# Kernel optimization log

Measured on AMD Instinct MI355X. Metric: run time of the kernel, lower is better.

Reference implementation:

```python
import jax, jax.numpy as jnp
import numpy as np
import math

B, T, C = 2, 4096, 768
NH = 12
HS = C // NH

def setup_inputs() -> dict:
    key = jax.random.key(0)
    k1, k2, k3 = jax.random.split(key, 3)
    x = jax.random.normal(k1, (B, T, C), dtype=jnp.float32)
    w_attn = jax.random.normal(k2, (C, 3 * C), dtype=jnp.float32) * (1.0 / math.sqrt(C))
    w_proj = jax.random.normal(k3, (C, C), dtype=jnp.float32) * (1.0 / math.sqrt(C))
    return {"x": x, "w_attn": w_attn, "w_proj": w_proj}

def reference(x, w_attn, w_proj):
    b, t, c = x.shape
    qkv = x @ w_attn                      # [b, t, 3c]
    q, k, v = jnp.split(qkv, 3, axis=-1)
    # [b, nh, t, hs]
    q = q.reshape(b, t, NH, HS).transpose(0, 2, 1, 3)
    k = k.reshape(b, t, NH, HS).transpose(0, 2, 1, 3)
    v = v.reshape(b, t, NH, HS).transpose(0, 2, 1, 3)
    scores = jnp.einsum('bhqd,bhkd->bhqk', q, k) / math.sqrt(HS)
    causal = jnp.tril(jnp.ones((t, t), dtype=bool))
    scores = jnp.where(causal[None, None], scores, -jnp.inf)
    att = jax.nn.softmax(scores, axis=-1)  # dropout p=0 -> identity
    out = jnp.einsum('bhqk,bhkd->bhqd', att, v)
    out = out.transpose(0, 2, 1, 3).reshape(b, t, c)
    return out @ w_proj
```

## Files before the change

kernel.cpp:

```cpp
#include <hip/hip_runtime.h>
#include <hip/hip_bf16.h>
#include <stdint.h>

#define NB 2
#define NT 4096
#define NC 768
#define NHEAD 12
#define HS 64
#define MTOK (NB * NT)
#define C3 (3 * NC)

typedef __bf16 bf16x8 __attribute__((ext_vector_type(8)));
typedef float f32x4 __attribute__((ext_vector_type(4)));
typedef float f32x16 __attribute__((ext_vector_type(16)));

#define KSCALE_LOG2E 0.18033688011f

__device__ __forceinline__ unsigned short f2bf(float f) {
  union { float f; uint32_t u; } v; v.f = f;
  uint32_t r = v.u + 0x7fffu + ((v.u >> 16) & 1u);
  return (unsigned short)(r >> 16);
}
__device__ __forceinline__ unsigned short bft(float f) {
  return (unsigned short)(__builtin_bit_cast(unsigned int, f) >> 16);
}
__device__ __forceinline__ uint32_t pack_bf2(float a, float b) {
  return __builtin_amdgcn_perm(__builtin_bit_cast(uint32_t, a),
                               __builtin_bit_cast(uint32_t, b), 0x03020706u);
}

__device__ __forceinline__ void gload_lds16(const unsigned short* g, unsigned short* ldsbase) {
  __builtin_amdgcn_global_load_lds(
      (const __attribute__((address_space(1))) unsigned int*)g,
      (__attribute__((address_space(3))) unsigned int*)ldsbase, 16, 0, 0);
}

__device__ __forceinline__ f32x4 mfma16(bf16x8 a, bf16x8 b, f32x4 c) {
  return __builtin_amdgcn_mfma_f32_16x16x32_bf16(a, b, c, 0, 0, 0);
}
__device__ __forceinline__ f32x16 mfma32(bf16x8 a, bf16x8 b, f32x16 c) {
  return __builtin_amdgcn_mfma_f32_32x32x16_bf16(a, b, c, 0, 0, 0);
}

__global__ __launch_bounds__(256) void prep(
    const float* __restrict__ x, const float* __restrict__ wa, const float* __restrict__ wp,
    unsigned short* __restrict__ xb, unsigned short* __restrict__ waT,
    unsigned short* __restrict__ wpT) {
  const int bx = blockIdx.x;
  if (bx < 576) {
    __shared__ float tile[64][65];
    const float* src; unsigned short* dst;
    int srcN, dstN, k0, n0, qscale;
    if (bx < 432) {
      src = wa; dst = waT; srcN = C3; dstN = NC; qscale = 1;
      k0 = (bx / 36) * 64; n0 = (bx % 36) * 64;
    } else {
      const int t = bx - 432;
      src = wp; dst = wpT; srcN = NC; dstN = NC; qscale = 0;
      k0 = (t / 12) * 64; n0 = (t % 12) * 64;
    }
    const int tr = threadIdx.x >> 4;
    const int tc = (threadIdx.x & 15) * 4;
#pragma unroll
    for (int p = 0; p < 4; ++p) {
      const int r = p * 16 + tr;
      const float4 v = *reinterpret_cast<const float4*>(src + (size_t)(k0 + r) * srcN + n0 + tc);
      tile[r][tc + 0] = v.x; tile[r][tc + 1] = v.y;
      tile[r][tc + 2] = v.z; tile[r][tc + 3] = v.w;
    }
    __syncthreads();
#pragma unroll
    for (int p = 0; p < 4; ++p) {
      const int n = p * 16 + tr;
      const float sc = (qscale && (n0 + n) < NC) ? KSCALE_LOG2E : 1.0f;
      ushort4 o;
      o.x = f2bf(tile[tc + 0][n] * sc); o.y = f2bf(tile[tc + 1][n] * sc);
      o.z = f2bf(tile[tc + 2][n] * sc); o.w = f2bf(tile[tc + 3][n] * sc);
      *reinterpret_cast<ushort4*>(dst + (size_t)(n0 + n) * dstN + k0 + tc) = o;
    }
  } else {
    const int gid = (bx - 576) * 256 + threadIdx.x;
    const float4 v = reinterpret_cast<const float4*>(x)[gid];
    ushort4 o;
    o.x = f2bf(v.x); o.y = f2bf(v.y); o.z = f2bf(v.z); o.w = f2bf(v.w);
    reinterpret_cast<ushort4*>(xb)[gid] = o;
  }
}

template <int OUT_BF16>
__global__ __launch_bounds__(256) void gemm128(
    const unsigned short* __restrict__ A,
    const unsigned short* __restrict__ Bt,
    void* __restrict__ Cout,
    unsigned short* __restrict__ vT,
    int M, int N, int K) {
  __shared__ unsigned short smem[2 * 128 * 64];
  unsigned short* As = smem;
  unsigned short* Bs = smem + 128 * 64;

  const int tid = threadIdx.x;
  const int wave = tid >> 6;
  const int lane = tid & 63;
  const int li = lane & 15;
  const int lq = lane >> 4;
  const int wm = wave & 1;
  const int wn = wave >> 1;
  const int row0 = blockIdx.y * 128;
  const int col0 = blockIdx.x * 128;

  const int crow = lane >> 3;
  const int cchunk = ((lane & 7) ^ crow) * 8;

  f32x4 acc[4][4] = {};

  for (int k0 = 0; k0 < K; k0 += 64) {
#pragma unroll
    for (int i = 0; i < 4; ++i) {
      const int R = wave * 32 + i * 8;
      gload_lds16(A + (size_t)(row0 + R + crow) * K + k0 + cchunk, &As[R * 64]);
      gload_lds16(Bt + (size_t)(col0 + R + crow) * K + k0 + cchunk, &Bs[R * 64]);
    }
    __syncthreads();

#pragma unroll
    for (int ks = 0; ks < 2; ++ks) {
      bf16x8 af[4], bf[4];
#pragma unroll
      for (int f = 0; f < 4; ++f) {
        const int arow = wm * 64 + f * 16 + li;
        af[f] = *reinterpret_cast<const bf16x8*>(&As[arow * 64 + (((ks * 4 + lq) ^ (li & 7)) << 3)]);
        const int brow = wn * 64 + f * 16 + li;
        bf[f] = *reinterpret_cast<const bf16x8*>(&Bs[brow * 64 + (((ks * 4 + lq) ^ (li & 7)) << 3)]);
      }
#pragma unroll
      for (int fa = 0; fa < 4; ++fa)
#pragma unroll
        for (int fb = 0; fb < 4; ++fb)
          acc[fa][fb] = mfma16(af[fa], bf[fb], acc[fa][fb]);
    }
    __syncthreads();
  }

  if (OUT_BF16) {
    if (col0 >= 2 * NC) {
      const int b = row0 >> 12;
      const int t0r = row0 & (NT - 1);
      const int h0 = (col0 - 2 * NC) >> 6;
#pragma unroll
      for (int fa = 0; fa < 4; ++fa) {
#pragma unroll
        for (int fb = 0; fb < 4; ++fb) {
          const int cc = wn * 64 + fb * 16 + li;
#pragma unroll
          for (int r = 0; r < 4; ++r) {
            const int tt = wm * 64 + fa * 16 + lq * 4 + r;
            const int slot = cc * 16 + ((tt >> 3) ^ (cc & 15));
            smem[slot * 8 + (tt & 7)] = f2bf(acc[fa][fb][r]);
          }
        }
      }
      __syncthreads();
      const int ch = tid & 15;
#pragma unroll
      for (int j = 0; j < 8; ++j) {
        const int cc = (tid >> 4) + 16 * j;
        const uint4 v = *reinterpret_cast<const uint4*>(
            smem + (size_t)(cc * 16 + (ch ^ (cc & 15))) * 8);
        const int bh = b * NHEAD + h0 + (cc >> 6);
        const int d = cc & 63;
        *reinterpret_cast<uint4*>(vT + (size_t)bh * HS * NT + (size_t)d * NT + t0r + ch * 8) = v;
      }
    } else {
      unsigned short* Cb = (unsigned short*)Cout;
#pragma unroll
      for (int fa = 0; fa < 4; ++fa) {
        const int gr = row0 + wm * 64 + fa * 16 + lq * 4;
#pragma unroll
        for (int fb = 0; fb < 4; ++fb) {
          const int gc = col0 + wn * 64 + fb * 16 + li;
#pragma unroll
          for (int r = 0; r < 4; ++r)
            Cb[(size_t)(gr + r) * N + gc] = f2bf(acc[fa][fb][r]);
        }
      }
    }
  } else {
    float* Cf = (float*)Cout;
#pragma unroll
    for (int fa = 0; fa < 4; ++fa) {
      const int gr = row0 + wm * 64 + fa * 16 + lq * 4;
#pragma unroll
      for (int fb = 0; fb < 4; ++fb) {
        const int gc = col0 + wn * 64 + fb * 16 + li;
#pragma unroll
        for (int r = 0; r < 4; ++r)
          Cf[(size_t)(gr + r) * N + gc] = acc[fa][fb][r];
      }
    }
  }
}


__device__ const uint8_t g_items[48] = {
  95,127,15, 94,126, 93,125,14, 92,124, 91,123,13, 90,122, 89,121,12, 88,120,
  87,119,11, 86,118, 85,117,10, 84,116, 83,115,9, 82,114, 81,113,8, 80,112,
  7,6,5,4,3,2,1,0};

__global__ __launch_bounds__(256) void attn(
    const unsigned short* __restrict__ qkv,
    const unsigned short* __restrict__ vT,
    float* __restrict__ Oacc,
    float* __restrict__ lacc,
    unsigned short* __restrict__ aob) {
  __shared__ unsigned short Ks[3][64 * 64];
  __shared__ unsigned short Vts[3][64 * 64];

  const int tid = threadIdx.x;
  const int wave = tid >> 6;
  const int lane = tid & 63;
  const int l31 = lane & 31;
  const int lh = lane >> 5;
  const int sw = l31 & 7;

  const int bid = (int)blockIdx.x;
  const int xcd = bid & 7;
  const int wl = bid >> 3;
  const int grp = xcd * 3 + wl % 3;
  const int e = (int)g_items[wl / 3];
  const int qi = e & 31;
  const int part = (e >> 5) & 1;
  const int split = e >> 6;
  const int nt = 2 * qi + 2;
  int tauS, tauE;
  if (split) { if (part) { tauS = nt >> 1; tauE = nt; } else { tauS = 0; tauE = nt >> 1; } }
  else       { tauS = 0; tauE = nt; }
  const int b = grp / 12;
  const int h = grp - b * 12;
  const int q0 = qi * 128;
  const int bh = grp;

  const size_t baseQ = (size_t)b * NT * C3 + (size_t)h * HS;
  const size_t baseK = baseQ + NC;
  const unsigned short* kq = qkv + baseK;
  const unsigned short* vbase = vT + (size_t)bh * HS * NT;

  const int qw = q0 + wave * 32;
  const int qtok = qw + l31;

  bf16x8 bq[4];
#pragma unroll
  for (int ks = 0; ks < 4; ++ks)
    bq[ks] = *reinterpret_cast<const bf16x8*>(
        qkv + baseQ + (size_t)(qw + l31) * C3 + ks * 16 + lh * 8);

  bf16x8 vones;
#pragma unroll
  for (int i = 0; i < 8; ++i) vones[i] = (__bf16)1.0f;

  f32x16 o0 = {}, o1 = {}, la = {};
  const f32x16 zf = {};

  const int grow = lane >> 3;
  const int gch = (lane & 7) ^ grow;
  const int wr0 = wave * 8;
  const int wr1 = wave * 8 + 32;

#define STAGE(TAU, BUFI)                                                        \
  do {                                                                          \
    const int t0s_ = (TAU) * 64;                                                \
    gload_lds16(kq + (size_t)(t0s_ + wr0 + grow) * C3 + gch * 8,                \
                &Ks[BUFI][wr0 * 64]);                                           \
    gload_lds16(kq + (size_t)(t0s_ + wr1 + grow) * C3 + gch * 8,                \
                &Ks[BUFI][wr1 * 64]);                                           \
    gload_lds16(vbase + (size_t)(wr0 + grow) * NT + t0s_ + gch * 8,             \
                &Vts[BUFI][wr0 * 64]);                                          \
    gload_lds16(vbase + (size_t)(wr1 + grow) * NT + t0s_ + gch * 8,             \
                &Vts[BUFI][wr1 * 64]);                                          \
  } while (0)

#define EXP_PACK(ST, KBLK, DOMASK)                                             \
  do {                                                                         \
    const int kb_ = t0 + (KBLK) * 32 + 4 * lh;                                 \
    float p_[16];                                                              \
    _Pragma("unroll") for (int r = 0; r < 16; ++r) {                           \
      float v_ = (ST)[r];                                                      \
      if (DOMASK) {                                                            \
        const int kt_ = kb_ + (r & 3) + 8 * (r >> 2);                          \
        if (kt_ > qtok) v_ = -INFINITY;                                        \
      }                                                                        \
      p_[r] = __builtin_amdgcn_exp2f(v_);                                      \
    }                                                                          \
    _Pragma("unroll") for (int s = 0; s < 2; ++s) {                            \
      uint32_t a_ = pack_bf2(p_[8 * s + 0], p_[8 * s + 1]);                    \
      uint32_t b_ = pack_bf2(p_[8 * s + 2], p_[8 * s + 3]);                    \
      uint32_t c_ = pack_bf2(p_[8 * s + 4], p_[8 * s + 5]);                    \
      uint32_t d_ = pack_bf2(p_[8 * s + 6], p_[8 * s + 7]);                    \
      asm("v_permlane32_swap_b32 %0, %1" : "+v"(a_), "+v"(c_));                \
      asm("v_permlane32_swap_b32 %0, %1" : "+v"(b_), "+v"(d_));                \
      union { uint32_t u[4]; bf16x8 v8; } pu_;                                 \
      pu_.u[0] = a_; pu_.u[1] = b_; pu_.u[2] = c_; pu_.u[3] = d_;              \
      pa[2 * (KBLK) + s] = pu_.v8;                                             \
    }                                                                          \
  } while (0)

#define PV_STEP(KS)                                                            \
  do {                                                                         \
    const int off_ = ((((KS) * 2 + lh) ^ sw) << 3);                            \
    const bf16x8 bv0_ =                                                        \
        *reinterpret_cast<const bf16x8*>(Vc + (size_t)l31 * 64 + off_);        \
    const bf16x8 bv1_ =                                                        \
        *reinterpret_cast<const bf16x8*>(Vc + (size_t)(32 + l31) * 64 + off_); \
    la = mfma32(pa[KS], vones, la);                                            \
    o0 = mfma32(pa[KS], bv0_, o0);                                             \
    o1 = mfma32(pa[KS], bv1_, o1);                                             \
  } while (0)

  STAGE(tauS, 0);
  STAGE(tauS + 1, 1);

  int cur = 0;
  for (int tau = tauS; tau < tauE; ++tau) {
    const int t0 = tau * 64;
    if (tau + 1 < tauE) asm volatile("s_waitcnt vmcnt(4)" ::: "memory");
    else                asm volatile("s_waitcnt vmcnt(0)" ::: "memory");
    __builtin_amdgcn_s_barrier();
    __builtin_amdgcn_sched_barrier(0);
    if (tau + 2 < tauE) {
      int nb = cur + 2; if (nb >= 3) nb -= 3;
      STAGE(tau + 2, nb);
    }

    const unsigned short* Kc = Ks[cur];
    const unsigned short* Vc = Vts[cur];

    if (t0 <= qw + 31) {
      const bool act1 = (t0 + 32 <= qw + 31);
      const bool m0 = (t0 + 31 > qw);
      const bool m1 = (t0 + 63 > qw);

      f32x16 st0, st1;
      __builtin_amdgcn_s_setprio(1);
      {
        const bf16x8 ka0 = *reinterpret_cast<const bf16x8*>(
            Kc + (size_t)l31 * 64 + ((lh ^ sw) << 3));
        st0 = mfma32(ka0, bq[0], zf);
      }
#pragma unroll
      for (int ks = 1; ks < 4; ++ks) {
        const bf16x8 ka = *reinterpret_cast<const bf16x8*>(
            Kc + (size_t)l31 * 64 + (((ks * 2 + lh) ^ sw) << 3));
        st0 = mfma32(ka, bq[ks], st0);
      }
      if (act1) {
        {
          const bf16x8 ka0 = *reinterpret_cast<const bf16x8*>(
              Kc + (size_t)(32 + l31) * 64 + ((lh ^ sw) << 3));
          st1 = mfma32(ka0, bq[0], zf);
        }
#pragma unroll
        for (int ks = 1; ks < 4; ++ks) {
          const bf16x8 ka = *reinterpret_cast<const bf16x8*>(
              Kc + (size_t)(32 + l31) * 64 + (((ks * 2 + lh) ^ sw) << 3));
          st1 = mfma32(ka, bq[ks], st1);
        }
      }
      __builtin_amdgcn_s_setprio(0);

      bf16x8 pa[4];
      if (m0) EXP_PACK(st0, 0, 1); else EXP_PACK(st0, 0, 0);
      if (act1) {
        if (m1) EXP_PACK(st1, 1, 1); else EXP_PACK(st1, 1, 0);
      }

      __builtin_amdgcn_s_setprio(1);
      PV_STEP(0); PV_STEP(1);
      if (act1) { PV_STEP(2); PV_STEP(3); }
      __builtin_amdgcn_s_setprio(0);
    }
    ++cur; if (cur == 3) cur = 0;
  }
#undef STAGE
#undef EXP_PACK
#undef PV_STEP

  if (split) {
    float* lrow = lacc + (size_t)bh * NT;
#pragma unroll
    for (int r = 0; r < 16; ++r) {
      const int q = qw + (r & 3) + 8 * (r >> 2) + 4 * lh;
      const int srow = part ? (q - 2048) : q;
      if (l31 == 0) lrow[srow] = la[r];
      float* orow = Oacc + ((size_t)b * NT + srow) * NC + h * HS;
      orow[l31] = o0[r];
      orow[32 + l31] = o1[r];
    }
  } else {
#pragma unroll
    for (int r = 0; r < 16; ++r) {
      const int q = qw + (r & 3) + 8 * (r >> 2) + 4 * lh;
      const float inv = 1.0f / la[r];
      unsigned short* orow = aob + ((size_t)b * NT + q) * NC + h * HS;
      orow[l31] = bft(o0[r] * inv);
      orow[32 + l31] = bft(o1[r] * inv);
    }
  }
}

__global__ __launch_bounds__(256) void finalize(
    const float* __restrict__ Oacc, const float* __restrict__ lacc,
    unsigned short* __restrict__ aob) {
  const int idx4 = (blockIdx.x * 256 + threadIdx.x);
  if (idx4 >= NB * (NT / 2) * NC / 4) return;
  const int idx = idx4 * 4;
  const int rowp = idx / NC;
  const int cc = idx - rowp * NC;
  const int b = rowp >> 11;
  const int t = (NT / 2) + (rowp & 2047);
  const int h = cc >> 6;
  const float* lrow = lacc + (size_t)(b * NHEAD + h) * NT;
  const float inv = 1.0f / (lrow[t] + lrow[t - 2048]);
  const size_t base0 = ((size_t)b * NT + t) * NC + cc;
  const size_t base1 = ((size_t)b * NT + (t - 2048)) * NC + cc;
  const float4 v0 = *reinterpret_cast<const float4*>(Oacc + base0);
  const float4 v1 = *reinterpret_cast<const float4*>(Oacc + base1);
  ushort4 o;
  o.x = bft((v0.x + v1.x) * inv); o.y = bft((v0.y + v1.y) * inv);
  o.z = bft((v0.z + v1.z) * inv); o.w = bft((v0.w + v1.w) * inv);
  *reinterpret_cast<ushort4*>(aob + base0) = o;
}

extern "C" void kernel_launch(void* const* d_in, const int* in_sizes, int n_in,
                              void* d_out, int out_size, void* d_ws, size_t ws_size,
                              hipStream_t stream) {
  const float* x = (const float*)d_in[0];
  const float* w_attn = (const float*)d_in[1];
  const float* w_proj = (const float*)d_in[2];
  float* outp = (float*)d_out;

  char* w = (char*)d_ws;
  float* Oacc = (float*)w;
  unsigned short* xb = (unsigned short*)w;
  unsigned short* waT = xb + (size_t)MTOK * NC;
  float* lacc = Oacc + (size_t)MTOK * NC;
  unsigned short* qkvb = (unsigned short*)(lacc + (size_t)NB * NHEAD * NT);
  unsigned short* aob  = qkvb + (size_t)MTOK * C3;
  unsigned short* vTb  = aob + (size_t)MTOK * NC;
  unsigned short* wpT  = vTb + (size_t)MTOK * NC;

  prep<<<576 + MTOK * NC / 4 / 256, 256, 0, stream>>>(x, w_attn, w_proj, xb, waT, wpT);

  gemm128<1><<<dim3(C3 / 128, MTOK / 128), 256, 0, stream>>>(xb, waT, qkvb, vTb, MTOK, C3, NC);

  attn<<<1152, 256, 0, stream>>>(qkvb, vTb, Oacc, lacc, aob);

  finalize<<<(NB * (NT / 2) * NC / 4 + 255) / 256, 256, 0, stream>>>(Oacc, lacc, aob);

  gemm128<0><<<dim3(NC / 128, MTOK / 128), 256, 0, stream>>>(aob, wpT, outp, nullptr, MTOK, NC, NC);
}
```

Measured before the change: 242.3 us.

## Split causal attention into fixed 8-tile key chunks merged with atomic adds

Replaces the hand-built 48-entry work table, which split only the largest query tiles in two, with an arithmetic mapping that cuts every query tile into chunks of up to 8 key tiles. This triples the grid to 3456 blocks for better load balance across CUs. Partial outputs and row sums from tiles with more than one chunk are merged through float atomicAdd into a zeroed accumulator. The cost is an added memset of the accumulator, a large volume of global atomics, and a finalize pass that now covers most tokens instead of half.

```diff
diff --git a/kernel.cpp b/kernel.cpp
--- a/kernel.cpp
+++ b/kernel.cpp
@@ -201,11 +201,6 @@
 }
 
 
-__device__ const uint8_t g_items[48] = {
-  95,127,15, 94,126, 93,125,14, 92,124, 91,123,13, 90,122, 89,121,12, 88,120,
-  87,119,11, 86,118, 85,117,10, 84,116, 83,115,9, 82,114, 81,113,8, 80,112,
-  7,6,5,4,3,2,1,0};
-
 __global__ __launch_bounds__(256) void attn(
     const unsigned short* __restrict__ qkv,
     const unsigned short* __restrict__ vT,
@@ -226,17 +221,22 @@
   const int xcd = bid & 7;
   const int wl = bid >> 3;
   const int grp = xcd * 3 + wl % 3;
-  const int e = (int)g_items[wl / 3];
-  const int qi = e & 31;
-  const int part = (e >> 5) & 1;
-  const int split = e >> 6;
-  const int nt = 2 * qi + 2;
-  int tauS, tauE;
-  if (split) { if (part) { tauS = nt >> 1; tauE = nt; } else { tauS = 0; tauE = nt >> 1; } }
-  else       { tauS = 0; tauE = nt; }
+  const int c = 143 - wl / 3;
+  int g = 0;
+#pragma unroll
+  for (int gg = 1; gg < 8; ++gg)
+    if (2 * gg * (gg + 1) <= c) g = gg;
+  const int rem = c - 2 * g * (g + 1);
+  const int dq = rem / (g + 1);
+  const int qi = 4 * g + dq;
+  const int ck = rem - dq * (g + 1);
+  const int q0 = qi * 128;
+  const int ntile = 2 * qi + 2;
+  const int tauS = ck * 8;
+  const int tauE = (tauS + 8 < ntile) ? tauS + 8 : ntile;
+  const int direct = (qi <= 3);
   const int b = grp / 12;
   const int h = grp - b * 12;
-  const int q0 = qi * 128;
   const int bh = grp;
 
   const size_t baseQ = (size_t)b * NT * C3 + (size_t)h * HS;
@@ -383,16 +383,15 @@
 #undef EXP_PACK
 #undef PV_STEP
 
-  if (split) {
+  if (!direct) {
+    const size_t obase = (size_t)b * NT * NC + (size_t)h * HS;
     float* lrow = lacc + (size_t)bh * NT;
 #pragma unroll
     for (int r = 0; r < 16; ++r) {
       const int q = qw + (r & 3) + 8 * (r >> 2) + 4 * lh;
-      const int srow = part ? (q - 2048) : q;
-      if (l31 == 0) lrow[srow] = la[r];
-      float* orow = Oacc + ((size_t)b * NT + srow) * NC + h * HS;
-      orow[l31] = o0[r];
-      orow[32 + l31] = o1[r];
+      if (l31 == 0) atomicAdd(&lrow[q], la[r]);
+      atomicAdd(&Oacc[obase + (size_t)q * NC + l31], o0[r]);
+      atomicAdd(&Oacc[obase + (size_t)q * NC + 32 + l31], o1[r]);
     }
   } else {
 #pragma unroll
@@ -410,23 +409,20 @@
     const float* __restrict__ Oacc, const float* __restrict__ lacc,
     unsigned short* __restrict__ aob) {
   const int idx4 = (blockIdx.x * 256 + threadIdx.x);
-  if (idx4 >= NB * (NT / 2) * NC / 4) return;
+  if (idx4 >= NB * (NT - 512) * NC / 4) return;
   const int idx = idx4 * 4;
   const int rowp = idx / NC;
   const int cc = idx - rowp * NC;
-  const int b = rowp >> 11;
-  const int t = (NT / 2) + (rowp & 2047);
+  const int b = (rowp >= (NT - 512)) ? 1 : 0;
+  const int t = 512 + rowp - b * (NT - 512);
   const int h = cc >> 6;
-  const float* lrow = lacc + (size_t)(b * NHEAD + h) * NT;
-  const float inv = 1.0f / (lrow[t] + lrow[t - 2048]);
-  const size_t base0 = ((size_t)b * NT + t) * NC + cc;
-  const size_t base1 = ((size_t)b * NT + (t - 2048)) * NC + cc;
-  const float4 v0 = *reinterpret_cast<const float4*>(Oacc + base0);
-  const float4 v1 = *reinterpret_cast<const float4*>(Oacc + base1);
+  const float inv = 1.0f / lacc[(size_t)(b * NHEAD + h) * NT + t];
+  const size_t base = ((size_t)b * NT + t) * NC + cc;
+  const float4 v = *reinterpret_cast<const float4*>(Oacc + base);
   ushort4 o;
-  o.x = bft((v0.x + v1.x) * inv); o.y = bft((v0.y + v1.y) * inv);
-  o.z = bft((v0.z + v1.z) * inv); o.w = bft((v0.w + v1.w) * inv);
-  *reinterpret_cast<ushort4*>(aob + base0) = o;
+  o.x = bft(v.x * inv); o.y = bft(v.y * inv);
+  o.z = bft(v.z * inv); o.w = bft(v.w * inv);
+  *reinterpret_cast<ushort4*>(aob + base) = o;
 }
 
 extern "C" void kernel_launch(void* const* d_in, const int* in_sizes, int n_in,
@@ -451,9 +447,11 @@
 
   gemm128<1><<<dim3(C3 / 128, MTOK / 128), 256, 0, stream>>>(xb, waT, qkvb, vTb, MTOK, C3, NC);
 
-  attn<<<1152, 256, 0, stream>>>(qkvb, vTb, Oacc, lacc, aob);
-
-  finalize<<<(NB * (NT / 2) * NC / 4 + 255) / 256, 256, 0, stream>>>(Oacc, lacc, aob);
+  hipMemsetAsync(Oacc, 0, ((size_t)MTOK * NC + (size_t)NB * NHEAD * NT) * sizeof(float), stream);
+
+  attn<<<3456, 256, 0, stream>>>(qkvb, vTb, Oacc, lacc, aob);
+
+  finalize<<<(NB * (NT - 512) * NC / 4 + 255) / 256, 256, 0, stream>>>(Oacc, lacc, aob);
 
   gemm128<0><<<dim3(NC / 128, MTOK / 128), 256, 0, stream>>>(aob, wpT, outp, nullptr, MTOK, NC, NC);
 }
```

Result: slower. 311.3 us (+28.5%).

## Split every causal attention row-block into two halves and store only Q/K

Applied to the files above, without the earlier changes.

Attention work is now split uniformly: every 128-query block is cut into two KV halves, which replaces the old table that split only the longest blocks. The launch grows from 1152 to 1536 blocks, and each half writes fp32 partial outputs and row sums into separate buffers. The second partial buffer reuses the final output buffer as scratch. The QKV GEMM now writes only Q and K with a narrower row stride, since V is already stored transposed, which shrinks the qkv buffer. The cost is that finalize must now merge partials for all tokens, so it reads and writes more fp32 data, and the attention kernel stores every output in fp32.

```diff
diff --git a/kernel.cpp b/kernel.cpp
--- a/kernel.cpp
+++ b/kernel.cpp
@@ -9,6 +9,7 @@
 #define HS 64
 #define MTOK (NB * NT)
 #define C3 (3 * NC)
+#define CQK (2 * NC)
 
 typedef __bf16 bf16x8 __attribute__((ext_vector_type(8)));
 typedef float f32x4 __attribute__((ext_vector_type(4)));
@@ -93,7 +94,7 @@
     const unsigned short* __restrict__ Bt,
     void* __restrict__ Cout,
     unsigned short* __restrict__ vT,
-    int M, int N, int K) {
+    int M, int N, int K, int ldc) {
   __shared__ unsigned short smem[2 * 128 * 64];
   unsigned short* As = smem;
   unsigned short* Bs = smem + 128 * 64;
@@ -180,7 +181,7 @@
           const int gc = col0 + wn * 64 + fb * 16 + li;
 #pragma unroll
           for (int r = 0; r < 4; ++r)
-            Cb[(size_t)(gr + r) * N + gc] = f2bf(acc[fa][fb][r]);
+            Cb[(size_t)(gr + r) * ldc + gc] = f2bf(acc[fa][fb][r]);
         }
       }
     }
@@ -194,24 +195,20 @@
         const int gc = col0 + wn * 64 + fb * 16 + li;
 #pragma unroll
         for (int r = 0; r < 4; ++r)
-          Cf[(size_t)(gr + r) * N + gc] = acc[fa][fb][r];
+          Cf[(size_t)(gr + r) * ldc + gc] = acc[fa][fb][r];
       }
     }
   }
 }
 
-
-__device__ const uint8_t g_items[48] = {
-  95,127,15, 94,126, 93,125,14, 92,124, 91,123,13, 90,122, 89,121,12, 88,120,
-  87,119,11, 86,118, 85,117,10, 84,116, 83,115,9, 82,114, 81,113,8, 80,112,
-  7,6,5,4,3,2,1,0};
 
 __global__ __launch_bounds__(256) void attn(
     const unsigned short* __restrict__ qkv,
     const unsigned short* __restrict__ vT,
-    float* __restrict__ Oacc,
-    float* __restrict__ lacc,
-    unsigned short* __restrict__ aob) {
+    float* __restrict__ OpartA,
+    float* __restrict__ OpartB,
+    float* __restrict__ laccA,
+    float* __restrict__ laccB) {
   __shared__ unsigned short Ks[3][64 * 64];
   __shared__ unsigned short Vts[3][64 * 64];
 
@@ -226,20 +223,18 @@
   const int xcd = bid & 7;
   const int wl = bid >> 3;
   const int grp = xcd * 3 + wl % 3;
-  const int e = (int)g_items[wl / 3];
-  const int qi = e & 31;
-  const int part = (e >> 5) & 1;
-  const int split = e >> 6;
+  const int rank = wl / 3;
+  const int qi = 31 - (rank >> 1);
+  const int part = rank & 1;
   const int nt = 2 * qi + 2;
-  int tauS, tauE;
-  if (split) { if (part) { tauS = nt >> 1; tauE = nt; } else { tauS = 0; tauE = nt >> 1; } }
-  else       { tauS = 0; tauE = nt; }
+  const int tauS = part ? 0 : (qi + 1);
+  const int tauE = part ? (qi + 1) : nt;
   const int b = grp / 12;
   const int h = grp - b * 12;
   const int q0 = qi * 128;
   const int bh = grp;
 
-  const size_t baseQ = (size_t)b * NT * C3 + (size_t)h * HS;
+  const size_t baseQ = (size_t)b * NT * CQK + (size_t)h * HS;
   const size_t baseK = baseQ + NC;
   const unsigned short* kq = qkv + baseK;
   const unsigned short* vbase = vT + (size_t)bh * HS * NT;
@@ -251,7 +246,7 @@
 #pragma unroll
   for (int ks = 0; ks < 4; ++ks)
     bq[ks] = *reinterpret_cast<const bf16x8*>(
-        qkv + baseQ + (size_t)(qw + l31) * C3 + ks * 16 + lh * 8);
+        qkv + baseQ + (size_t)(qw + l31) * CQK + ks * 16 + lh * 8);
 
   bf16x8 vones;
 #pragma unroll
@@ -268,9 +263,9 @@
 #define STAGE(TAU, BUFI)                                                        \
   do {                                                                          \
     const int t0s_ = (TAU) * 64;                                                \
-    gload_lds16(kq + (size_t)(t0s_ + wr0 + grow) * C3 + gch * 8,                \
+    gload_lds16(kq + (size_t)(t0s_ + wr0 + grow) * CQK + gch * 8,               \
                 &Ks[BUFI][wr0 * 64]);                                           \
-    gload_lds16(kq + (size_t)(t0s_ + wr1 + grow) * C3 + gch * 8,                \
+    gload_lds16(kq + (size_t)(t0s_ + wr1 + grow) * CQK + gch * 8,               \
                 &Ks[BUFI][wr1 * 64]);                                           \
     gload_lds16(vbase + (size_t)(wr0 + grow) * NT + t0s_ + gch * 8,             \
                 &Vts[BUFI][wr0 * 64]);                                          \
@@ -383,50 +378,38 @@
 #undef EXP_PACK
 #undef PV_STEP
 
-  if (split) {
-    float* lrow = lacc + (size_t)bh * NT;
-#pragma unroll
-    for (int r = 0; r < 16; ++r) {
-      const int q = qw + (r & 3) + 8 * (r >> 2) + 4 * lh;
-      const int srow = part ? (q - 2048) : q;
-      if (l31 == 0) lrow[srow] = la[r];
-      float* orow = Oacc + ((size_t)b * NT + srow) * NC + h * HS;
-      orow[l31] = o0[r];
-      orow[32 + l31] = o1[r];
-    }
-  } else {
-#pragma unroll
-    for (int r = 0; r < 16; ++r) {
-      const int q = qw + (r & 3) + 8 * (r >> 2) + 4 * lh;
-      const float inv = 1.0f / la[r];
-      unsigned short* orow = aob + ((size_t)b * NT + q) * NC + h * HS;
-      orow[l31] = bft(o0[r] * inv);
-      orow[32 + l31] = bft(o1[r] * inv);
-    }
+  float* slotO = part ? OpartB : OpartA;
+  float* lrow = (part ? laccB : laccA) + (size_t)bh * NT;
+#pragma unroll
+  for (int r = 0; r < 16; ++r) {
+    const int q = qw + (r & 3) + 8 * (r >> 2) + 4 * lh;
+    if (l31 == 0) lrow[q] = la[r];
+    float* orow = slotO + ((size_t)b * NT + q) * NC + h * HS;
+    orow[l31] = o0[r];
+    orow[32 + l31] = o1[r];
   }
 }
 
 __global__ __launch_bounds__(256) void finalize(
-    const float* __restrict__ Oacc, const float* __restrict__ lacc,
+    const float* __restrict__ OpartA, const float* __restrict__ OpartB,
+    const float* __restrict__ laccA, const float* __restrict__ laccB,
     unsigned short* __restrict__ aob) {
   const int idx4 = (blockIdx.x * 256 + threadIdx.x);
-  if (idx4 >= NB * (NT / 2) * NC / 4) return;
+  if (idx4 >= MTOK * NC / 4) return;
   const int idx = idx4 * 4;
-  const int rowp = idx / NC;
-  const int cc = idx - rowp * NC;
-  const int b = rowp >> 11;
-  const int t = (NT / 2) + (rowp & 2047);
+  const int row = idx / NC;
+  const int cc = idx - row * NC;
+  const int b = row >> 12;
+  const int t = row & (NT - 1);
   const int h = cc >> 6;
-  const float* lrow = lacc + (size_t)(b * NHEAD + h) * NT;
-  const float inv = 1.0f / (lrow[t] + lrow[t - 2048]);
-  const size_t base0 = ((size_t)b * NT + t) * NC + cc;
-  const size_t base1 = ((size_t)b * NT + (t - 2048)) * NC + cc;
-  const float4 v0 = *reinterpret_cast<const float4*>(Oacc + base0);
-  const float4 v1 = *reinterpret_cast<const float4*>(Oacc + base1);
+  const size_t lofs = (size_t)(b * NHEAD + h) * NT + t;
+  const float inv = 1.0f / (laccA[lofs] + laccB[lofs]);
+  const float4 v0 = *reinterpret_cast<const float4*>(OpartA + (size_t)idx);
+  const float4 v1 = *reinterpret_cast<const float4*>(OpartB + (size_t)idx);
   ushort4 o;
   o.x = bft((v0.x + v1.x) * inv); o.y = bft((v0.y + v1.y) * inv);
   o.z = bft((v0.z + v1.z) * inv); o.w = bft((v0.w + v1.w) * inv);
-  *reinterpret_cast<ushort4*>(aob + base0) = o;
+  reinterpret_cast<ushort4*>(aob)[idx4] = o;
 }
 
 extern "C" void kernel_launch(void* const* d_in, const int* in_sizes, int n_in,
@@ -438,22 +421,25 @@
   float* outp = (float*)d_out;
 
   char* w = (char*)d_ws;
-  float* Oacc = (float*)w;
+  float* OpartA = (float*)w;
   unsigned short* xb = (unsigned short*)w;
   unsigned short* waT = xb + (size_t)MTOK * NC;
-  float* lacc = Oacc + (size_t)MTOK * NC;
-  unsigned short* qkvb = (unsigned short*)(lacc + (size_t)NB * NHEAD * NT);
-  unsigned short* aob  = qkvb + (size_t)MTOK * C3;
+  float* laccA = OpartA + (size_t)MTOK * NC;
+  float* laccB = laccA + (size_t)NB * NHEAD * NT;
+  unsigned short* qkvb = (unsigned short*)(laccB + (size_t)NB * NHEAD * NT);
+  unsigned short* aob  = qkvb + (size_t)MTOK * CQK;
   unsigned short* vTb  = aob + (size_t)MTOK * NC;
   unsigned short* wpT  = vTb + (size_t)MTOK * NC;
 
   prep<<<576 + MTOK * NC / 4 / 256, 256, 0, stream>>>(x, w_attn, w_proj, xb, waT, wpT);
 
-  gemm128<1><<<dim3(C3 / 128, MTOK / 128), 256, 0, stream>>>(xb, waT, qkvb, vTb, MTOK, C3, NC);
-
-  attn<<<1152, 256, 0, stream>>>(qkvb, vTb, Oacc, lacc, aob);
-
-  finalize<<<(NB * (NT / 2) * NC / 4 + 255) / 256, 256, 0, stream>>>(Oacc, lacc, aob);
-
-  gemm128<0><<<dim3(NC / 128, MTOK / 128), 256, 0, stream>>>(aob, wpT, outp, nullptr, MTOK, NC, NC);
-}
+  gemm128<1><<<dim3(C3 / 128, MTOK / 128), 256, 0, stream>>>(
+      xb, waT, qkvb, vTb, MTOK, C3, NC, CQK);
+
+  attn<<<1536, 256, 0, stream>>>(qkvb, vTb, OpartA, outp, laccA, laccB);
+
+  finalize<<<(MTOK * NC / 4 + 255) / 256, 256, 0, stream>>>(OpartA, outp, laccA, laccB, aob);
+
+  gemm128<0><<<dim3(NC / 128, MTOK / 128), 256, 0, stream>>>(
+      aob, wpT, outp, nullptr, MTOK, NC, NC, NC);
+}
```

New measurement: 229.4 us. -5.3%, faster.
